# Performance work log

Hardware: AMD Instinct MI355X
Metric: run time of the kernel (lower is better)

## Reference

```python
import jax, jax.numpy as jnp
import numpy as np

B, T, D, H = 4, 2048, 1024, 16
DK = D // H

def setup_inputs() -> dict:
    key = jax.random.key(0)
    k1, k2, k3 = jax.random.split(key, 3)
    x = jax.random.normal(k1, (B, T, D), dtype=jnp.float32)
    w_qkv = jax.random.normal(k2, (D, 3 * D), dtype=jnp.float32) * (1.0 / np.sqrt(D))
    w_proj = jax.random.normal(k3, (D, D), dtype=jnp.float32) * (1.0 / np.sqrt(D))
    # additive causal mask: 0 on/below diagonal, -inf above
    neg = jnp.finfo(jnp.float32).min
    attn_mask = jnp.where(jnp.tril(jnp.ones((T, T), dtype=bool)), 0.0, neg)[None, None]
    return {"x": x, "attn_mask": attn_mask, "w_qkv": w_qkv, "w_proj": w_proj}


def reference(x, attn_mask, w_qkv, w_proj):
    Bx, Tx, Dx = x.shape
    qkv = x @ w_qkv                                  # [B,T,3D]
    q, k, v = jnp.split(qkv, 3, axis=-1)
    # [B,T,D] -> [B,H,T,dk]
    def to_heads(t):
        return t.reshape(Bx, Tx, H, DK).transpose(0, 2, 1, 3)
    q, k, v = to_heads(q), to_heads(k), to_heads(v)
    attn = jnp.einsum("bhqd,bhkd->bhqk", q, k) / jnp.sqrt(jnp.float32(DK))
    attn = attn + attn_mask
    attn = jax.nn.softmax(attn, axis=-1)
    out = jnp.einsum("bhqk,bhkd->bhqd", attn, v)     # [B,H,T,dk]
    out = out.transpose(0, 2, 1, 3).reshape(Bx, Tx, Dx)
    return out @ w_proj
```

## Files before the change

### kernel.cpp

```cpp
#include <hip/hip_runtime.h>
#include <hip/hip_bf16.h>
#include <stdint.h>

typedef __bf16 bf16x8 __attribute__((ext_vector_type(8)));
typedef __bf16 bf16x4 __attribute__((ext_vector_type(4)));
typedef float  f32x4  __attribute__((ext_vector_type(4)));

__device__ __forceinline__ void gl_lds16(const void* g, void* l) {
  __builtin_amdgcn_global_load_lds(
      (const __attribute__((address_space(1))) unsigned int*)g,
      (__attribute__((address_space(3))) unsigned int*)l, 16, 0, 0);
}

__global__ __launch_bounds__(256) void convert_x(
    const float* __restrict__ src, __bf16* __restrict__ dst) {
  const size_t i = ((size_t)blockIdx.x * 256 + threadIdx.x) * 8;
  float4 v0 = *reinterpret_cast<const float4*>(src + i);
  float4 v1 = *reinterpret_cast<const float4*>(src + i + 4);
  bf16x8 o;
  o[0] = (__bf16)v0.x; o[1] = (__bf16)v0.y; o[2] = (__bf16)v0.z; o[3] = (__bf16)v0.w;
  o[4] = (__bf16)v1.x; o[5] = (__bf16)v1.y; o[6] = (__bf16)v1.z; o[7] = (__bf16)v1.w;
  *reinterpret_cast<bf16x8*>(dst + i) = o;
}

__global__ __launch_bounds__(256) void transpose_convert(
    const float* __restrict__ src, __bf16* __restrict__ dst, int K, int N) {
  __shared__ __bf16 tile[64][65];
  const int n0 = blockIdx.x * 64, k0 = blockIdx.y * 64;
  const int t = threadIdx.x;
#pragma unroll
  for (int e = 0; e < 16; ++e) {
    int idx = e * 256 + t;
    int kk = idx >> 6, nn = idx & 63;
    tile[nn][kk] = (__bf16)src[(size_t)(k0 + kk) * N + n0 + nn];
  }
  __syncthreads();
#pragma unroll
  for (int e = 0; e < 16; ++e) {
    int idx = e * 256 + t;
    int nn = idx >> 6, kk = idx & 63;
    dst[(size_t)(n0 + nn) * K + k0 + kk] = tile[nn][kk];
  }
}

__device__ __forceinline__ void gemm_core_1024(
    const __bf16* __restrict__ Ag, const __bf16* __restrict__ Bg,
    int m0, int n0, __bf16* lds, f32x4 (&acc)[8][4]) {
  const int tid = threadIdx.x;
  const int wv = tid >> 6, l = tid & 63, g = l >> 4, lr = l & 15;
  const int sswL = (lr & 3) ^ ((lr >> 2) & 3);

  int arow[2], acol[2], brow[4], bcol[4];
#pragma unroll
  for (int e = 0; e < 2; ++e) {
    int c = e * 256 + tid, row = c >> 2, slot = c & 3;
    arow[e] = row;
    acol[e] = (slot ^ ((row & 3) ^ ((row >> 2) & 3))) * 8;
  }
#pragma unroll
  for (int e = 0; e < 4; ++e) {
    int c = e * 256 + tid, row = c >> 2, slot = c & 3;
    brow[e] = row;
    bcol[e] = (slot ^ ((row & 3) ^ ((row >> 2) & 3))) * 8;
  }

  auto STAGE = [&](int bufb, int t) {
    const int kb = t * 32;
#pragma unroll
    for (int e = 0; e < 2; ++e)
      gl_lds16(Ag + (size_t)(m0 + arow[e]) * 1024 + kb + acol[e],
               lds + bufb + (e * 256 + wv * 64) * 8);
#pragma unroll
    for (int e = 0; e < 4; ++e)
      gl_lds16(Bg + (size_t)(n0 + brow[e]) * 1024 + kb + bcol[e],
               lds + bufb + 4096 + (e * 256 + wv * 64) * 8);
  };

  int cur = 0, nx = 12288, nn = 24576;
  STAGE(cur, 0);
  STAGE(nx, 1);

#pragma unroll 1
  for (int t = 0; t < 32; ++t) {
    if (t < 31) asm volatile("s_waitcnt vmcnt(6)" ::: "memory");
    else        asm volatile("s_waitcnt vmcnt(0)" ::: "memory");
    __builtin_amdgcn_s_barrier();
    __builtin_amdgcn_sched_barrier(0);
    if (t + 2 < 32) STAGE(nn, t + 2);

    const char* Ab = (const char*)(lds + cur);
    const char* Bb = (const char*)(lds + cur + 4096);
    bf16x8 a[8], b[4];
#pragma unroll
    for (int mf = 0; mf < 8; ++mf)
      a[mf] = *reinterpret_cast<const bf16x8*>(
          Ab + (mf * 16 + lr) * 64 + ((g ^ sswL) << 4));
#pragma unroll
    for (int nf = 0; nf < 4; ++nf)
      b[nf] = *reinterpret_cast<const bf16x8*>(
          Bb + (wv * 64 + nf * 16 + lr) * 64 + ((g ^ sswL) << 4));
    __builtin_amdgcn_s_setprio(1);
#pragma unroll
    for (int mf = 0; mf < 8; ++mf)
#pragma unroll
      for (int nf = 0; nf < 4; ++nf)
        acc[mf][nf] = __builtin_amdgcn_mfma_f32_16x16x32_bf16(
            a[mf], b[nf], acc[mf][nf], 0, 0, 0);
    __builtin_amdgcn_s_setprio(0);

    int tmp = cur; cur = nx; nx = nn; nn = tmp;
  }
}

__global__ __launch_bounds__(256, 2) void qkv_gemm(
    const __bf16* __restrict__ Xb, const __bf16* __restrict__ WT,
    __bf16* __restrict__ Qb, __bf16* __restrict__ Kb, __bf16* __restrict__ Vb) {
  __shared__ __bf16 lds[36864];
  const int lin = blockIdx.x;
  const int sw = (lin & 7) * 96 + (lin >> 3);
  const int rb = sw / 12, cb = sw % 12;
  const int m0 = rb * 128, n0 = cb * 256;

  f32x4 acc[8][4] = {};
  gemm_core_1024(Xb, WT, m0, n0, lds, acc);

  const int tid = threadIdx.x, wv = tid >> 6, l = tid & 63, g = l >> 4, lr = l & 15;
  const int which = cb >> 2;

  if (which == 2) {
#pragma unroll
    for (int mf = 0; mf < 8; ++mf)
#pragma unroll
      for (int nf = 0; nf < 4; ++nf) {
        int m_ = m0 + mf * 16 + g * 4;
        int n  = n0 + wv * 64 + nf * 16 + lr;
        int hc = n & 1023, hh = hc >> 6, dk = hc & 63;
        int bbv = m_ >> 11, tt = m_ & 2047;
        bf16x4 vk;
        vk[0] = (__bf16)acc[mf][nf][0]; vk[1] = (__bf16)acc[mf][nf][1];
        vk[2] = (__bf16)acc[mf][nf][2]; vk[3] = (__bf16)acc[mf][nf][3];
        *reinterpret_cast<bf16x4*>(
            &Vb[((size_t)(bbv * 16 + hh) * 64 + dk) * 2048 + tt]) = vk;
      }
  } else if (which == 0) {
#pragma unroll
    for (int mf = 0; mf < 8; ++mf)
#pragma unroll
      for (int nf = 0; nf < 4; ++nf) {
        int m_ = m0 + mf * 16 + g * 4;
        int n  = n0 + wv * 64 + nf * 16 + lr;
        int hc = n & 1023, hh = hc >> 6, dk = hc & 63;
        int bbv = m_ >> 11, tt = m_ & 2047;
#pragma unroll
        for (int j = 0; j < 4; ++j)
          Qb[(((size_t)(bbv * 16 + hh)) * 2048 + tt + j) * 64 + dk] =
              (__bf16)(acc[mf][nf][j] * 0.18033688f);
      }
  } else {
#pragma unroll
    for (int mf = 0; mf < 8; ++mf)
#pragma unroll
      for (int nf = 0; nf < 4; ++nf) {
        int m_ = m0 + mf * 16 + g * 4;
        int n  = n0 + wv * 64 + nf * 16 + lr;
        int hc = n & 1023, hh = hc >> 6, dk = hc & 63;
        int bbv = m_ >> 11, tt = m_ & 2047;
#pragma unroll
        for (int j = 0; j < 4; ++j)
          Kb[(((size_t)(bbv * 16 + hh)) * 2048 + tt + j) * 64 + dk] =
              (__bf16)acc[mf][nf][j];
      }
  }
}

__global__ __launch_bounds__(256, 2) void proj_gemm(
    const __bf16* __restrict__ A, const __bf16* __restrict__ WT,
    float* __restrict__ Out) {
  __shared__ __bf16 lds[36864];
  const int lin = blockIdx.x;
  const int sw = (lin & 7) * 32 + (lin >> 3);
  const int rb = sw >> 2, cb = sw & 3;
  const int m0 = rb * 128, n0 = cb * 256;

  f32x4 acc[8][4] = {};
  gemm_core_1024(A, WT, m0, n0, lds, acc);

  const int tid = threadIdx.x, wv = tid >> 6, l = tid & 63, g = l >> 4, lr = l & 15;
#pragma unroll
  for (int mf = 0; mf < 8; ++mf)
#pragma unroll
    for (int nf = 0; nf < 4; ++nf) {
      int m_ = m0 + mf * 16 + g * 4;
      int n  = n0 + wv * 64 + nf * 16 + lr;
#pragma unroll
      for (int j = 0; j < 4; ++j)
        Out[(size_t)(m_ + j) * 1024 + n] = acc[mf][nf][j];
    }
}

__global__ __launch_bounds__(256, 2) void attn_kernel(
    const __bf16* __restrict__ Qb, const __bf16* __restrict__ Kb,
    const __bf16* __restrict__ VTb, __bf16* __restrict__ Ob) {
  __shared__ __bf16 Ks[2][4096];
  __shared__ __bf16 Vs[2][4096];
  __shared__ __bf16 PlA[4][1024];
  __shared__ __bf16 PlB[4][1024];
  const int t = threadIdx.x, l = t & 63, w = t >> 6;
  const int g = l >> 4, lr = l & 15;
  const int bid = blockIdx.x;
  const int logical = (bid & 7) * 64 + (bid >> 3);
  const int pj = logical & 7, bh = logical >> 3;
  const int bb = bh >> 4, h = bh & 15;
  const __bf16* Kbase = Kb  + (size_t)bh * 2048 * 64;
  const __bf16* Vbase = VTb + (size_t)bh * 64 * 2048;
  const __bf16* Qbase = Qb  + (size_t)bh * 2048 * 64;
  const int swz = (lr & 7) << 4;

  int cur = 0;
#pragma unroll 1
  for (int phase = 0; phase < 2; ++phase) {
    const int J = phase ? (15 - pj) : pj;
    const int qtA = 2 * J, qtB = 2 * J + 1;
    const int qrowA = J * 128 + w * 16 + lr;
    const int qrowB = qrowA + 64;
    const bf16x8 qfA0 = *reinterpret_cast<const bf16x8*>(Qbase + (size_t)qrowA * 64 + g * 8);
    const bf16x8 qfA1 = *reinterpret_cast<const bf16x8*>(Qbase + (size_t)qrowA * 64 + 32 + g * 8);
    const bf16x8 qfB0 = *reinterpret_cast<const bf16x8*>(Qbase + (size_t)qrowB * 64 + g * 8);
    const bf16x8 qfB1 = *reinterpret_cast<const bf16x8*>(Qbase + (size_t)qrowB * 64 + 32 + g * 8);

    f32x4 otA[4] = {}, otB[4] = {};
    float lsA = 0.f, lsB = 0.f;

#pragma unroll
    for (int rep = 0; rep < 2; ++rep) {
      int c = w * 128 + rep * 64 + l;
      int row = c >> 3, cc = c & 7;
      int pc = (cc ^ (row & 7)) * 8;
      gl_lds16(Kbase + (size_t)row * 64 + pc, &Ks[cur][(w * 128 + rep * 64) * 8]);
      gl_lds16(Vbase + (size_t)row * 2048 + pc, &Vs[cur][(w * 128 + rep * 64) * 8]);
    }
    __syncthreads();

    for (int kt = 0; kt <= qtB; ++kt) {
      const bool aAct = (kt <= qtA);
      if (kt < qtB) {
        const int nv0 = (kt + 1) * 64;
#pragma unroll
        for (int rep = 0; rep < 2; ++rep) {
          int c = w * 128 + rep * 64 + l;
          int row = c >> 3, cc = c & 7;
          int pc = (cc ^ (row & 7)) * 8;
          gl_lds16(Kbase + (size_t)(nv0 + row) * 64 + pc,
                   &Ks[cur ^ 1][(w * 128 + rep * 64) * 8]);
          gl_lds16(Vbase + (size_t)row * 2048 + nv0 + pc,
                   &Vs[cur ^ 1][(w * 128 + rep * 64) * 8]);
        }
      }
      bf16x8 klo[4], khi[4];
#pragma unroll
      for (int nf = 0; nf < 4; ++nf) {
        const char* kr = (const char*)&Ks[cur][(nf * 16 + lr) * 64];
        klo[nf] = *reinterpret_cast<const bf16x8*>(kr + ((g * 16) ^ swz));
        khi[nf] = *reinterpret_cast<const bf16x8*>(kr + ((64 + g * 16) ^ swz));
      }
      f32x4 stA[4], stB[4];
      __builtin_amdgcn_s_setprio(1);
#pragma unroll
      for (int nf = 0; nf < 4; ++nf) {
        f32x4 z = {};
        z = __builtin_amdgcn_mfma_f32_16x16x32_bf16(klo[nf], qfB0, z, 0, 0, 0);
        stB[nf] = __builtin_amdgcn_mfma_f32_16x16x32_bf16(khi[nf], qfB1, z, 0, 0, 0);
      }
      if (aAct) {
#pragma unroll
        for (int nf = 0; nf < 4; ++nf) {
          f32x4 z = {};
          z = __builtin_amdgcn_mfma_f32_16x16x32_bf16(klo[nf], qfA0, z, 0, 0, 0);
          stA[nf] = __builtin_amdgcn_mfma_f32_16x16x32_bf16(khi[nf], qfA1, z, 0, 0, 0);
        }
      }
      __builtin_amdgcn_s_setprio(0);
      if (kt == qtB) {
#pragma unroll
        for (int nf = 0; nf < 4; ++nf)
#pragma unroll
          for (int j = 0; j < 4; ++j)
            if (nf * 16 + g * 4 + j > w * 16 + lr) stB[nf][j] = -INFINITY;
      }
      if (aAct && kt == qtA) {
#pragma unroll
        for (int nf = 0; nf < 4; ++nf)
#pragma unroll
          for (int j = 0; j < 4; ++j)
            if (nf * 16 + g * 4 + j > w * 16 + lr) stA[nf][j] = -INFINITY;
      }
      {
        float rs = 0.f;
        char* prow = (char*)&PlB[w][lr * 64];
#pragma unroll
        for (int nf = 0; nf < 4; ++nf) {
#pragma unroll
          for (int j = 0; j < 4; ++j) {
            float p = __builtin_amdgcn_exp2f(stB[nf][j]);
            stB[nf][j] = p;
            rs += p;
          }
          bf16x4 pk;
          pk[0] = (__bf16)stB[nf][0]; pk[1] = (__bf16)stB[nf][1];
          pk[2] = (__bf16)stB[nf][2]; pk[3] = (__bf16)stB[nf][3];
          *reinterpret_cast<bf16x4*>(prow + ((nf * 32 + g * 8) ^ swz)) = pk;
        }
        lsB += rs;
      }
      if (aAct) {
        float rs = 0.f;
        char* prow = (char*)&PlA[w][lr * 64];
#pragma unroll
        for (int nf = 0; nf < 4; ++nf) {
#pragma unroll
          for (int j = 0; j < 4; ++j) {
            float p = __builtin_amdgcn_exp2f(stA[nf][j]);
            stA[nf][j] = p;
            rs += p;
          }
          bf16x4 pk;
          pk[0] = (__bf16)stA[nf][0]; pk[1] = (__bf16)stA[nf][1];
          pk[2] = (__bf16)stA[nf][2]; pk[3] = (__bf16)stA[nf][3];
          *reinterpret_cast<bf16x4*>(prow + ((nf * 32 + g * 8) ^ swz)) = pk;
        }
        lsA += rs;
      }
      {
        bf16x8 vlo[4], vhi[4];
#pragma unroll
        for (int nf = 0; nf < 4; ++nf) {
          const char* vr = (const char*)&Vs[cur][(nf * 16 + lr) * 64];
          vlo[nf] = *reinterpret_cast<const bf16x8*>(vr + ((g * 16) ^ swz));
          vhi[nf] = *reinterpret_cast<const bf16x8*>(vr + ((64 + g * 16) ^ swz));
        }
        const char* prB = (const char*)&PlB[w][lr * 64];
        bf16x8 pb0 = *reinterpret_cast<const bf16x8*>(prB + ((g * 16) ^ swz));
        bf16x8 pb1 = *reinterpret_cast<const bf16x8*>(prB + ((64 + g * 16) ^ swz));
        __builtin_amdgcn_s_setprio(1);
#pragma unroll
        for (int nf = 0; nf < 4; ++nf) {
          otB[nf] = __builtin_amdgcn_mfma_f32_16x16x32_bf16(vlo[nf], pb0, otB[nf], 0, 0, 0);
          otB[nf] = __builtin_amdgcn_mfma_f32_16x16x32_bf16(vhi[nf], pb1, otB[nf], 0, 0, 0);
        }
        __builtin_amdgcn_s_setprio(0);
        if (aAct) {
          const char* prA = (const char*)&PlA[w][lr * 64];
          bf16x8 pa0 = *reinterpret_cast<const bf16x8*>(prA + ((g * 16) ^ swz));
          bf16x8 pa1 = *reinterpret_cast<const bf16x8*>(prA + ((64 + g * 16) ^ swz));
          __builtin_amdgcn_s_setprio(1);
#pragma unroll
          for (int nf = 0; nf < 4; ++nf) {
            otA[nf] = __builtin_amdgcn_mfma_f32_16x16x32_bf16(vlo[nf], pa0, otA[nf], 0, 0, 0);
            otA[nf] = __builtin_amdgcn_mfma_f32_16x16x32_bf16(vhi[nf], pa1, otA[nf], 0, 0, 0);
          }
          __builtin_amdgcn_s_setprio(0);
        }
      }
      __syncthreads();
      cur ^= 1;
    }

    lsA += __shfl_xor(lsA, 16); lsA += __shfl_xor(lsA, 32);
    lsB += __shfl_xor(lsB, 16); lsB += __shfl_xor(lsB, 32);
    const float rlA = 1.f / lsA, rlB = 1.f / lsB;
#pragma unroll
    for (int nf = 0; nf < 4; ++nf) {
      bf16x4 ok;
      ok[0] = (__bf16)(otA[nf][0] * rlA); ok[1] = (__bf16)(otA[nf][1] * rlA);
      ok[2] = (__bf16)(otA[nf][2] * rlA); ok[3] = (__bf16)(otA[nf][3] * rlA);
      *reinterpret_cast<bf16x4*>(
          &Ob[((size_t)(bb * 2048 + qrowA)) * 1024 + h * 64 + nf * 16 + g * 4]) = ok;
      bf16x4 ok2;
      ok2[0] = (__bf16)(otB[nf][0] * rlB); ok2[1] = (__bf16)(otB[nf][1] * rlB);
      ok2[2] = (__bf16)(otB[nf][2] * rlB); ok2[3] = (__bf16)(otB[nf][3] * rlB);
      *reinterpret_cast<bf16x4*>(
          &Ob[((size_t)(bb * 2048 + qrowB)) * 1024 + h * 64 + nf * 16 + g * 4]) = ok2;
    }
  }
}

extern "C" void kernel_launch(void* const* d_in, const int* in_sizes, int n_in,
                              void* d_out, int out_size, void* d_ws, size_t ws_size,
                              hipStream_t stream) {
  const float* x      = (const float*)d_in[0];
  const float* w_qkv  = (const float*)d_in[2];
  const float* w_proj = (const float*)d_in[3];
  float* out = (float*)d_out;

  char* ws = (char*)d_ws;
  __bf16* wt_qkv  = (__bf16*)(ws);
  __bf16* wt_proj = (__bf16*)(ws + 6291456);
  __bf16* Qb      = (__bf16*)(ws + 8388608);
  __bf16* Kb      = (__bf16*)(ws + 8388608 + 16777216);
  __bf16* VTb     = (__bf16*)(ws + 8388608 + 2 * 16777216);
  __bf16* Ob      = (__bf16*)(ws + 8388608 + 3 * 16777216);
  __bf16* Xb      = Ob;

  convert_x<<<4096, 256, 0, stream>>>(x, Xb);
  transpose_convert<<<dim3(3072 / 64, 1024 / 64), 256, 0, stream>>>(w_qkv, wt_qkv, 1024, 3072);
  transpose_convert<<<dim3(1024 / 64, 1024 / 64), 256, 0, stream>>>(w_proj, wt_proj, 1024, 1024);
  qkv_gemm<<<768, 256, 0, stream>>>(Xb, wt_qkv, Qb, Kb, VTb);
  attn_kernel<<<512, 256, 0, stream>>>(Qb, Kb, VTb, Ob);
  proj_gemm<<<256, 256, 0, stream>>>(Ob, wt_proj, out);
}
```

Before: 163.5 us.

## Retile QKV and projection GEMMs for more blocks and merge prep kernels

The GEMM core is templated on the number of N fragments per wave. The QKV GEMM now uses 128x192 tiles (1024 blocks) and the projection GEMM 128x128 tiles (512 blocks), so both fill the GPU's CUs better. The QKV epilogue now selects Q, K or V per fragment because a tile can span the boundaries. The three input-conversion kernels are merged into a single launch to cut launch overhead. Smaller tiles lower arithmetic intensity and increase redundant A loads.

```diff
diff --git a/kernel.cpp b/kernel.cpp
--- a/kernel.cpp
+++ b/kernel.cpp
@@ -12,22 +12,33 @@
       (__attribute__((address_space(3))) unsigned int*)l, 16, 0, 0);
 }
 
-__global__ __launch_bounds__(256) void convert_x(
-    const float* __restrict__ src, __bf16* __restrict__ dst) {
-  const size_t i = ((size_t)blockIdx.x * 256 + threadIdx.x) * 8;
-  float4 v0 = *reinterpret_cast<const float4*>(src + i);
-  float4 v1 = *reinterpret_cast<const float4*>(src + i + 4);
-  bf16x8 o;
-  o[0] = (__bf16)v0.x; o[1] = (__bf16)v0.y; o[2] = (__bf16)v0.z; o[3] = (__bf16)v0.w;
-  o[4] = (__bf16)v1.x; o[5] = (__bf16)v1.y; o[6] = (__bf16)v1.z; o[7] = (__bf16)v1.w;
-  *reinterpret_cast<bf16x8*>(dst + i) = o;
-}
-
-__global__ __launch_bounds__(256) void transpose_convert(
-    const float* __restrict__ src, __bf16* __restrict__ dst, int K, int N) {
+__global__ __launch_bounds__(256) void prep_kernel(
+    const float* __restrict__ x, __bf16* __restrict__ Xb,
+    const float* __restrict__ w_qkv, __bf16* __restrict__ wt_qkv,
+    const float* __restrict__ w_proj, __bf16* __restrict__ wt_proj) {
   __shared__ __bf16 tile[64][65];
-  const int n0 = blockIdx.x * 64, k0 = blockIdx.y * 64;
-  const int t = threadIdx.x;
+  const int bid = blockIdx.x, t = threadIdx.x;
+  if (bid < 4096) {
+    const size_t i = ((size_t)bid * 256 + t) * 8;
+    float4 v0 = *reinterpret_cast<const float4*>(x + i);
+    float4 v1 = *reinterpret_cast<const float4*>(x + i + 4);
+    bf16x8 o;
+    o[0] = (__bf16)v0.x; o[1] = (__bf16)v0.y; o[2] = (__bf16)v0.z; o[3] = (__bf16)v0.w;
+    o[4] = (__bf16)v1.x; o[5] = (__bf16)v1.y; o[6] = (__bf16)v1.z; o[7] = (__bf16)v1.w;
+    *reinterpret_cast<bf16x8*>(Xb + i) = o;
+    return;
+  }
+  const float* src; __bf16* dst; int K, N, bx, by;
+  if (bid < 4864) {
+    int idx = bid - 4096;
+    src = w_qkv; dst = wt_qkv; K = 1024; N = 3072;
+    bx = idx % 48; by = idx / 48;
+  } else {
+    int idx = bid - 4864;
+    src = w_proj; dst = wt_proj; K = 1024; N = 1024;
+    bx = idx & 15; by = idx >> 4;
+  }
+  const int n0 = bx * 64, k0 = by * 64;
 #pragma unroll
   for (int e = 0; e < 16; ++e) {
     int idx = e * 256 + t;
@@ -43,14 +54,16 @@
   }
 }
 
+template <int NFRAG>
 __device__ __forceinline__ void gemm_core_1024(
     const __bf16* __restrict__ Ag, const __bf16* __restrict__ Bg,
-    int m0, int n0, __bf16* lds, f32x4 (&acc)[8][4]) {
+    int m0, int n0, __bf16* lds, f32x4 (&acc)[8][NFRAG]) {
+  constexpr int BUFSZ = 4096 + NFRAG * 2048;
   const int tid = threadIdx.x;
   const int wv = tid >> 6, l = tid & 63, g = l >> 4, lr = l & 15;
   const int sswL = (lr & 3) ^ ((lr >> 2) & 3);
 
-  int arow[2], acol[2], brow[4], bcol[4];
+  int arow[2], acol[2], brow[NFRAG], bcol[NFRAG];
 #pragma unroll
   for (int e = 0; e < 2; ++e) {
     int c = e * 256 + tid, row = c >> 2, slot = c & 3;
@@ -58,7 +71,7 @@
     acol[e] = (slot ^ ((row & 3) ^ ((row >> 2) & 3))) * 8;
   }
 #pragma unroll
-  for (int e = 0; e < 4; ++e) {
+  for (int e = 0; e < NFRAG; ++e) {
     int c = e * 256 + tid, row = c >> 2, slot = c & 3;
     brow[e] = row;
     bcol[e] = (slot ^ ((row & 3) ^ ((row >> 2) & 3))) * 8;
@@ -71,39 +84,43 @@
       gl_lds16(Ag + (size_t)(m0 + arow[e]) * 1024 + kb + acol[e],
                lds + bufb + (e * 256 + wv * 64) * 8);
 #pragma unroll
-    for (int e = 0; e < 4; ++e)
+    for (int e = 0; e < NFRAG; ++e)
       gl_lds16(Bg + (size_t)(n0 + brow[e]) * 1024 + kb + bcol[e],
                lds + bufb + 4096 + (e * 256 + wv * 64) * 8);
   };
 
-  int cur = 0, nx = 12288, nn = 24576;
+  int cur = 0, nx = BUFSZ, nn = 2 * BUFSZ;
   STAGE(cur, 0);
   STAGE(nx, 1);
 
 #pragma unroll 1
   for (int t = 0; t < 32; ++t) {
-    if (t < 31) asm volatile("s_waitcnt vmcnt(6)" ::: "memory");
-    else        asm volatile("s_waitcnt vmcnt(0)" ::: "memory");
+    if (t < 31) {
+      if constexpr (NFRAG == 3) asm volatile("s_waitcnt vmcnt(5)" ::: "memory");
+      else                      asm volatile("s_waitcnt vmcnt(4)" ::: "memory");
+    } else {
+      asm volatile("s_waitcnt vmcnt(0)" ::: "memory");
+    }
     __builtin_amdgcn_s_barrier();
     __builtin_amdgcn_sched_barrier(0);
     if (t + 2 < 32) STAGE(nn, t + 2);
 
     const char* Ab = (const char*)(lds + cur);
     const char* Bb = (const char*)(lds + cur + 4096);
-    bf16x8 a[8], b[4];
+    bf16x8 a[8], b[NFRAG];
 #pragma unroll
     for (int mf = 0; mf < 8; ++mf)
       a[mf] = *reinterpret_cast<const bf16x8*>(
           Ab + (mf * 16 + lr) * 64 + ((g ^ sswL) << 4));
 #pragma unroll
-    for (int nf = 0; nf < 4; ++nf)
+    for (int nf = 0; nf < NFRAG; ++nf)
       b[nf] = *reinterpret_cast<const bf16x8*>(
-          Bb + (wv * 64 + nf * 16 + lr) * 64 + ((g ^ sswL) << 4));
+          Bb + (wv * NFRAG * 16 + nf * 16 + lr) * 64 + ((g ^ sswL) << 4));
     __builtin_amdgcn_s_setprio(1);
 #pragma unroll
     for (int mf = 0; mf < 8; ++mf)
 #pragma unroll
-      for (int nf = 0; nf < 4; ++nf)
+      for (int nf = 0; nf < NFRAG; ++nf)
         acc[mf][nf] = __builtin_amdgcn_mfma_f32_16x16x32_bf16(
             a[mf], b[nf], acc[mf][nf], 0, 0, 0);
     __builtin_amdgcn_s_setprio(0);
@@ -115,83 +132,64 @@
 __global__ __launch_bounds__(256, 2) void qkv_gemm(
     const __bf16* __restrict__ Xb, const __bf16* __restrict__ WT,
     __bf16* __restrict__ Qb, __bf16* __restrict__ Kb, __bf16* __restrict__ Vb) {
-  __shared__ __bf16 lds[36864];
+  __shared__ __bf16 lds[30720];
   const int lin = blockIdx.x;
-  const int sw = (lin & 7) * 96 + (lin >> 3);
-  const int rb = sw / 12, cb = sw % 12;
-  const int m0 = rb * 128, n0 = cb * 256;
-
-  f32x4 acc[8][4] = {};
-  gemm_core_1024(Xb, WT, m0, n0, lds, acc);
+  const int sw = (lin & 7) * 128 + (lin >> 3);
+  const int rb = sw >> 4, cb = sw & 15;
+  const int m0 = rb * 128, n0 = cb * 192;
+
+  f32x4 acc[8][3] = {};
+  gemm_core_1024<3>(Xb, WT, m0, n0, lds, acc);
 
   const int tid = threadIdx.x, wv = tid >> 6, l = tid & 63, g = l >> 4, lr = l & 15;
-  const int which = cb >> 2;
-
-  if (which == 2) {
-#pragma unroll
-    for (int mf = 0; mf < 8; ++mf)
-#pragma unroll
-      for (int nf = 0; nf < 4; ++nf) {
-        int m_ = m0 + mf * 16 + g * 4;
-        int n  = n0 + wv * 64 + nf * 16 + lr;
-        int hc = n & 1023, hh = hc >> 6, dk = hc & 63;
-        int bbv = m_ >> 11, tt = m_ & 2047;
+#pragma unroll
+  for (int mf = 0; mf < 8; ++mf)
+#pragma unroll
+    for (int nf = 0; nf < 3; ++nf) {
+      int m_ = m0 + mf * 16 + g * 4;
+      int nb = n0 + wv * 48 + nf * 16;
+      int which = nb >> 10, hc = nb & 1023;
+      int hh = hc >> 6, dk0 = hc & 63;
+      int bbv = m_ >> 11, tt = m_ & 2047;
+      if (which == 2) {
         bf16x4 vk;
         vk[0] = (__bf16)acc[mf][nf][0]; vk[1] = (__bf16)acc[mf][nf][1];
         vk[2] = (__bf16)acc[mf][nf][2]; vk[3] = (__bf16)acc[mf][nf][3];
         *reinterpret_cast<bf16x4*>(
-            &Vb[((size_t)(bbv * 16 + hh) * 64 + dk) * 2048 + tt]) = vk;
-      }
-  } else if (which == 0) {
-#pragma unroll
-    for (int mf = 0; mf < 8; ++mf)
-#pragma unroll
-      for (int nf = 0; nf < 4; ++nf) {
-        int m_ = m0 + mf * 16 + g * 4;
-        int n  = n0 + wv * 64 + nf * 16 + lr;
-        int hc = n & 1023, hh = hc >> 6, dk = hc & 63;
-        int bbv = m_ >> 11, tt = m_ & 2047;
+            &Vb[((size_t)(bbv * 16 + hh) * 64 + dk0 + lr) * 2048 + tt]) = vk;
+      } else if (which == 0) {
 #pragma unroll
         for (int j = 0; j < 4; ++j)
-          Qb[(((size_t)(bbv * 16 + hh)) * 2048 + tt + j) * 64 + dk] =
+          Qb[(((size_t)(bbv * 16 + hh)) * 2048 + tt + j) * 64 + dk0 + lr] =
               (__bf16)(acc[mf][nf][j] * 0.18033688f);
-      }
-  } else {
-#pragma unroll
-    for (int mf = 0; mf < 8; ++mf)
-#pragma unroll
-      for (int nf = 0; nf < 4; ++nf) {
-        int m_ = m0 + mf * 16 + g * 4;
-        int n  = n0 + wv * 64 + nf * 16 + lr;
-        int hc = n & 1023, hh = hc >> 6, dk = hc & 63;
-        int bbv = m_ >> 11, tt = m_ & 2047;
+      } else {
 #pragma unroll
         for (int j = 0; j < 4; ++j)
-          Kb[(((size_t)(bbv * 16 + hh)) * 2048 + tt + j) * 64 + dk] =
+          Kb[(((size_t)(bbv * 16 + hh)) * 2048 + tt + j) * 64 + dk0 + lr] =
               (__bf16)acc[mf][nf][j];
       }
-  }
+    }
 }
 
 __global__ __launch_bounds__(256, 2) void proj_gemm(
     const __bf16* __restrict__ A, const __bf16* __restrict__ WT,
     float* __restrict__ Out) {
-  __shared__ __bf16 lds[36864];
+  __shared__ __bf16 lds[24576];
   const int lin = blockIdx.x;
-  const int sw = (lin & 7) * 32 + (lin >> 3);
-  const int rb = sw >> 2, cb = sw & 3;
-  const int m0 = rb * 128, n0 = cb * 256;
-
-  f32x4 acc[8][4] = {};
-  gemm_core_1024(A, WT, m0, n0, lds, acc);
+  const int sw = (lin & 7) * 64 + (lin >> 3);
+  const int rb = sw >> 3, cb = sw & 7;
+  const int m0 = rb * 128, n0 = cb * 128;
+
+  f32x4 acc[8][2] = {};
+  gemm_core_1024<2>(A, WT, m0, n0, lds, acc);
 
   const int tid = threadIdx.x, wv = tid >> 6, l = tid & 63, g = l >> 4, lr = l & 15;
 #pragma unroll
   for (int mf = 0; mf < 8; ++mf)
 #pragma unroll
-    for (int nf = 0; nf < 4; ++nf) {
+    for (int nf = 0; nf < 2; ++nf) {
       int m_ = m0 + mf * 16 + g * 4;
-      int n  = n0 + wv * 64 + nf * 16 + lr;
+      int n  = n0 + wv * 32 + nf * 16 + lr;
 #pragma unroll
       for (int j = 0; j < 4; ++j)
         Out[(size_t)(m_ + j) * 1024 + n] = acc[mf][nf][j];
@@ -401,10 +399,8 @@
   __bf16* Ob      = (__bf16*)(ws + 8388608 + 3 * 16777216);
   __bf16* Xb      = Ob;
 
-  convert_x<<<4096, 256, 0, stream>>>(x, Xb);
-  transpose_convert<<<dim3(3072 / 64, 1024 / 64), 256, 0, stream>>>(w_qkv, wt_qkv, 1024, 3072);
-  transpose_convert<<<dim3(1024 / 64, 1024 / 64), 256, 0, stream>>>(w_proj, wt_proj, 1024, 1024);
-  qkv_gemm<<<768, 256, 0, stream>>>(Xb, wt_qkv, Qb, Kb, VTb);
+  prep_kernel<<<5120, 256, 0, stream>>>(x, Xb, w_qkv, wt_qkv, w_proj, wt_proj);
+  qkv_gemm<<<1024, 256, 0, stream>>>(Xb, wt_qkv, Qb, Kb, VTb);
   attn_kernel<<<512, 256, 0, stream>>>(Qb, Kb, VTb, Ob);
-  proj_gemm<<<256, 256, 0, stream>>>(Ob, wt_proj, out);
-}
+  proj_gemm<<<512, 256, 0, stream>>>(Ob, wt_proj, out);
+}
```

Result: faster. 159.6 us (-2.4%).
